# Kernel tuning notes

Measured on AMD Instinct MI355X. Metric: run time of the kernel, lower is better.

The kernel has to match this reference:

```python
import jax, jax.numpy as jnp
import numpy as np

N_TRAIN, N_FEAT, N_HID, ENC = 4096, 64, 256, 256
N_ANTES, ATT_H, MAX_LEN = 2048, 256, 16


def setup_inputs() -> dict:
    key = jax.random.key(0)
    ks = jax.random.split(key, 8)
    s = 0.05
    f32 = jnp.float32
    return {
        "context": jax.random.normal(ks[0], (N_TRAIN, N_FEAT), f32),
        "S": jax.random.uniform(ks[1], (N_TRAIN, N_ANTES), dtype=f32),
        "enc_w1": s * jax.random.normal(ks[2], (N_HID, N_FEAT), f32),
        "enc_b1": jnp.zeros((N_HID,), f32),
        "enc_w2": s * jax.random.normal(ks[3], (ENC, N_HID), f32),
        "enc_b2": jnp.zeros((ENC,), f32),
        "w_ih": s * jax.random.normal(ks[4], (4 * ENC, N_ANTES), f32),
        "w_hh": s * jax.random.normal(ks[5], (4 * ENC, ENC), f32),
        "b_ih": jnp.zeros((4 * ENC,), f32),
        "b_hh": jnp.zeros((4 * ENC,), f32),
        "att_w1": s * jax.random.normal(ks[6], (ATT_H, N_TRAIN + ENC), f32),
        "att_b1": jnp.zeros((ATT_H,), f32),
        "att_w2": s * jax.random.normal(ks[7], (1, ATT_H), f32),
        "att_b2": jnp.zeros((1,), f32),
    }


def _forward(context, S, enc_w1, enc_b1, enc_w2, enc_b2,
             w_ih, w_hh, b_ih, b_hh, att_w1, att_b1, att_w2, att_b2):
    n_train, n_antes = S.shape
    # context encoder: Linear -> ReLU -> Linear, initializes LSTM hidden state
    phi = jax.nn.relu(context @ enc_w1.T + enc_b1) @ enc_w2.T + enc_b2  # [n_train, ENC]
    # attention first layer split: columns [:n_train] act on S.T rows, rest on e_t
    Wa, Wb = att_w1[:, :n_train], att_w1[:, n_train:]
    pre = S.T @ Wa.T  # [n_antes, ATT_H], constant across timesteps
    bias = b_ih + b_hh
    x0 = jnp.ones((n_train, n_antes), S.dtype)

    def step(carry, _):
        h, c, x = carry
        # one LSTM cell step (PyTorch gate order i, f, g, o)
        z = x @ w_ih.T + h @ w_hh.T + bias  # [n_train, 4*ENC]
        i, f, g, o = jnp.split(z, 4, axis=-1)
        c = jax.nn.sigmoid(f) * c + jax.nn.sigmoid(i) * jnp.tanh(g)
        h = jax.nn.sigmoid(o) * jnp.tanh(c)
        e_t = h.mean(axis=0)  # mean over n_train (torch e.mean(1) on [1,n_train,H])
        hid = jax.nn.relu(pre + e_t @ Wb.T + att_b1)  # [n_antes, ATT_H]
        scores = (hid @ att_w2.T + att_b2)[:, 0]      # [n_antes]
        logp = jax.nn.log_softmax(scores, axis=0)
        idx = jnp.argmax(logp)
        # next input: chosen antecedent column broadcast across all antecedents
        x_next = jnp.broadcast_to(S[:, idx][:, None], (n_train, n_antes))
        return (h, c, x_next), logp

    _, d = jax.lax.scan(jax.checkpoint(step), (phi, jnp.zeros_like(phi), x0),
                        None, length=MAX_LEN)
    return d  # [MAX_LEN, n_antes] == torch cat(...).transpose(0, 1)


def reference(context, S, enc_w1, enc_b1, enc_w2, enc_b2,
              w_ih, w_hh, b_ih, b_hh, att_w1, att_b1, att_w2, att_b2):
    return _forward(context, S, enc_w1, enc_b1, enc_w2, enc_b2,
                    w_ih, w_hh, b_ih, b_hh, att_w1, att_b1, att_w2, att_b2)
```

## Files before the change

kernel.cpp:

```cpp
#include <hip/hip_runtime.h>
#include <hip/hip_bf16.h>
#include <math.h>

#define N_TRAIN 4096
#define N_FEAT  64
#define N_HID   256
#define ENC     256
#define N_ANTES 2048
#define ATT_H   256
#define MAX_LEN 16

typedef unsigned int u32;
typedef unsigned short u16;
typedef short short8 __attribute__((ext_vector_type(8)));
typedef float floatx16 __attribute__((ext_vector_type(16)));

__device__ __forceinline__ float fsig(float x)  { return 1.f / (1.f + __expf(-x)); }
__device__ __forceinline__ float ftanh(float x) { return 2.f / (1.f + __expf(-2.f * x)) - 1.f; }

__device__ __forceinline__ u16 f2bf(float x) {
    u32 b = __float_as_uint(x);
    return (u16)((b + 0x7FFFu + ((b >> 16) & 1u)) >> 16);
}
__device__ __forceinline__ float bf2f(u16 h) {
    return __uint_as_float(((u32)h) << 16);
}
__device__ __forceinline__ void split_bf(float v, u16& hi, u16& lo) {
    u32 b = __float_as_uint(v);
    hi = (u16)(b >> 16);
    float r = v - __uint_as_float(b & 0xFFFF0000u);
    lo = (u16)(__float_as_uint(r) >> 16);
}

__device__ __forceinline__ int kin_of(int l, int j) {
    return ((l >> 5) << 2) + (j & 3) + ((j >> 2) << 3);
}

template <bool RELU>
__global__ __launch_bounds__(256) void gemm_abT(
    const float* __restrict__ A, const float* __restrict__ B,
    const float* __restrict__ bias, float* __restrict__ C,
    int M, int N, int K, int lda, int ldb, int ldc)
{
    __shared__ __align__(16) float As[16][68];
    __shared__ __align__(16) float Bs[16][68];
    const int tid = threadIdx.x;
    const int m0 = blockIdx.x * 64, n0 = blockIdx.y * 64;
    const int tx = tid & 15, ty = tid >> 4;
    const int kl = tid & 15, rl = tid >> 4;
    float acc[4][4] = {};

    for (int k0 = 0; k0 < K; k0 += 16) {
        #pragma unroll
        for (int pp = 0; pp < 4; ++pp) {
            int r = rl + pp * 16;
            As[kl][r] = A[(size_t)(m0 + r) * lda + k0 + kl];
            Bs[kl][r] = B[(size_t)(n0 + r) * ldb + k0 + kl];
        }
        __syncthreads();
        #pragma unroll
        for (int k = 0; k < 16; ++k) {
            float4 av = *(const float4*)&As[k][ty * 4];
            float4 bv = *(const float4*)&Bs[k][tx * 4];
            float a4[4] = {av.x, av.y, av.z, av.w};
            float b4[4] = {bv.x, bv.y, bv.z, bv.w};
            #pragma unroll
            for (int i = 0; i < 4; ++i)
                #pragma unroll
                for (int j = 0; j < 4; ++j)
                    acc[i][j] = fmaf(a4[i], b4[j], acc[i][j]);
        }
        __syncthreads();
    }
    #pragma unroll
    for (int i = 0; i < 4; ++i) {
        int m = m0 + ty * 4 + i;
        #pragma unroll
        for (int j = 0; j < 4; ++j) {
            int n = n0 + tx * 4 + j;
            float v = acc[i][j] + bias[n];
            if (RELU) v = fmaxf(v, 0.f);
            C[(size_t)m * ldc + n] = v;
        }
    }
}

__global__ __launch_bounds__(256) void k_rowsum(const float* __restrict__ w_ih,
                                                float* __restrict__ rowsum)
{
    __shared__ float red[256];
    const int j = blockIdx.x, tid = threadIdx.x;
    float s = 0.f;
    for (int i = tid; i < N_ANTES; i += 256) s += w_ih[(size_t)j * N_ANTES + i];
    red[tid] = s; __syncthreads();
    for (int off = 128; off > 0; off >>= 1) {
        if (tid < off) red[tid] += red[tid + off];
        __syncthreads();
    }
    if (tid == 0) rowsum[j] = red[0];
}

__global__ __launch_bounds__(256) void k_wbT(const float* __restrict__ att_w1,
                                             float* __restrict__ WbT)
{
    int gid = blockIdx.x * 256 + threadIdx.x;
    int j = gid >> 8, k = gid & 255;
    WbT[(size_t)k * 256 + j] = att_w1[(size_t)j * (N_TRAIN + ENC) + N_TRAIN + k];
}

__global__ __launch_bounds__(256) void k_packAf(const float* __restrict__ att_w1,
                                                u16* __restrict__ Af_hi,
                                                u16* __restrict__ Af_lo)
{
    int gid = blockIdx.x * 256 + threadIdx.x;
    int j  = gid & 7;
    int l  = (gid >> 3) & 63;
    int kt = (gid >> 9) & 255;
    int mt = gid >> 17;
    int m = mt * 32 + (l & 31);
    int k = kt * 16 + kin_of(l, j);
    float v = att_w1[(size_t)m * (N_TRAIN + ENC) + k];
    u16 hi, lo; split_bf(v, hi, lo);
    Af_hi[gid] = hi;
    Af_lo[gid] = lo;
}

#define PSPLIT 4
__global__ __launch_bounds__(256) void k_gemm_preT(
    const u16* __restrict__ Af_hi, const u16* __restrict__ Af_lo,
    const float* __restrict__ S, float* __restrict__ P)
{
    const int tid = threadIdx.x, lane = tid & 63, w = tid >> 6;
    const int kz = blockIdx.x;
    const int np = blockIdx.y;
    const int mq = blockIdx.z;
    const int mt = mq * 2 + (w & 1);
    const int ni = w >> 1;
    const int nb = np * 64 + ni * 32 + (lane & 31);
    const int kb = 4 * (lane >> 5);
    floatx16 acc = {0,0,0,0,0,0,0,0,0,0,0,0,0,0,0,0};

    const int kt_beg = kz * 64, kt_end = kt_beg + 64;
    #pragma unroll 4
    for (int kt = kt_beg; kt < kt_end; ++kt) {
        size_t ao = (((size_t)mt * 256 + kt) * 64 + lane) * 8;
        short8 ahi = *(const short8*)(Af_hi + ao);
        short8 alo = *(const short8*)(Af_lo + ao);
        short8 bhi, blo;
        #pragma unroll
        for (int j = 0; j < 8; ++j) {
            int k = kt * 16 + kb + (j & 3) + 8 * (j >> 2);
            float v = S[(size_t)k * N_ANTES + nb];
            u16 hi, lo; split_bf(v, hi, lo);
            bhi[j] = (short)hi;
            blo[j] = (short)lo;
        }
        acc = __builtin_amdgcn_mfma_f32_32x32x16_bf16(ahi, bhi, acc, 0, 0, 0);
        acc = __builtin_amdgcn_mfma_f32_32x32x16_bf16(ahi, blo, acc, 0, 0, 0);
        acc = __builtin_amdgcn_mfma_f32_32x32x16_bf16(alo, bhi, acc, 0, 0, 0);
    }

    float* Pk = P + (size_t)kz * (ATT_H * N_ANTES);
    #pragma unroll
    for (int q = 0; q < 16; ++q) {
        int row = mt * 32 + (q & 3) + 8 * (q >> 2) + 4 * (lane >> 5);
        Pk[(size_t)row * N_ANTES + nb] = acc[q];
    }
}

__global__ __launch_bounds__(256) void k_reduce4(const float* __restrict__ P,
                                                 float* __restrict__ preT)
{
    int gid = blockIdx.x * 256 + threadIdx.x;
    const int SZ = ATT_H * N_ANTES;
    preT[gid] = (P[gid] + P[gid + SZ]) + (P[gid + 2 * SZ] + P[gid + 3 * SZ]);
}

__global__ __launch_bounds__(256) void k_packWf(const float* __restrict__ w_hh,
                                                u16* __restrict__ Wf_hi,
                                                u16* __restrict__ Wf_lo)
{
    int gid = blockIdx.x * 256 + threadIdx.x;
    int j    = gid & 7;
    int l    = (gid >> 3) & 63;
    int kt   = (gid >> 9) & 15;
    int nsub = (gid >> 13) & 1;
    int cb   = gid >> 14;
    int k  = kt * 16 + kin_of(l, j);
    int cc = nsub * 32 + (l & 31);
    int jj = cb * 16 + (cc >> 2);
    int g  = cc & 3;
    int J  = g * 256 + jj;
    float v = w_hh[(size_t)J * 256 + k];
    u16 hi = f2bf(v);
    Wf_hi[gid] = hi;
    Wf_lo[gid] = f2bf(v - bf2f(hi));
}

__global__ __launch_bounds__(256) void k_packHf(const float* __restrict__ h,
                                                u16* __restrict__ Hf_hi,
                                                u16* __restrict__ Hf_lo)
{
    int gid = blockIdx.x * 256 + threadIdx.x;
    int j  = gid & 7;
    int l  = (gid >> 3) & 63;
    int kt = (gid >> 9) & 15;
    int mt = gid >> 13;
    int m = mt * 32 + (l & 31);
    int k = kt * 16 + kin_of(l, j);
    float v = h[(size_t)m * 256 + k];
    u16 hi = f2bf(v);
    Hf_hi[gid] = hi;
    Hf_lo[gid] = f2bf(v - bf2f(hi));
}

__global__ __launch_bounds__(256) void k_zgemm(
    const u16* __restrict__ Hf_hi_r, const u16* __restrict__ Hf_lo_r,
    u16* __restrict__ Hf_hi_w, u16* __restrict__ Hf_lo_w,
    const u16* __restrict__ Wf_hi, const u16* __restrict__ Wf_lo,
    float* __restrict__ c,
    const float* __restrict__ rowsum, const float* __restrict__ b_ih,
    const float* __restrict__ b_hh, const float* __restrict__ S,
    const int* __restrict__ idx_buf, int t, float* __restrict__ e_acc_t)
{
    __shared__ __align__(16) float z_lds[128][68];
    __shared__ float red[256];
    const int tid  = threadIdx.x;
    const int lane = tid & 63;
    const int msub = tid >> 6;
    const int rb = blockIdx.x;
    const int cb = blockIdx.y;
    const int mt = rb * 4 + msub;

    floatx16 acc0 = {0,0,0,0,0,0,0,0,0,0,0,0,0,0,0,0};
    floatx16 acc1 = {0,0,0,0,0,0,0,0,0,0,0,0,0,0,0,0};
    const size_t aoff  = (size_t)mt * 16 * 512 + lane * 8;
    const size_t boff0 = (size_t)(cb * 2 + 0) * 16 * 512 + lane * 8;
    const size_t boff1 = (size_t)(cb * 2 + 1) * 16 * 512 + lane * 8;

    #pragma unroll 4
    for (int kt = 0; kt < 16; ++kt) {
        short8 ahi = *(const short8*)(Hf_hi_r + aoff  + kt * 512);
        short8 alo = *(const short8*)(Hf_lo_r + aoff  + kt * 512);
        short8 b0h = *(const short8*)(Wf_hi   + boff0 + kt * 512);
        short8 b0l = *(const short8*)(Wf_lo   + boff0 + kt * 512);
        short8 b1h = *(const short8*)(Wf_hi   + boff1 + kt * 512);
        short8 b1l = *(const short8*)(Wf_lo   + boff1 + kt * 512);
        acc0 = __builtin_amdgcn_mfma_f32_32x32x16_bf16(ahi, b0h, acc0, 0, 0, 0);
        acc0 = __builtin_amdgcn_mfma_f32_32x32x16_bf16(ahi, b0l, acc0, 0, 0, 0);
        acc0 = __builtin_amdgcn_mfma_f32_32x32x16_bf16(alo, b0h, acc0, 0, 0, 0);
        acc1 = __builtin_amdgcn_mfma_f32_32x32x16_bf16(ahi, b1h, acc1, 0, 0, 0);
        acc1 = __builtin_amdgcn_mfma_f32_32x32x16_bf16(ahi, b1l, acc1, 0, 0, 0);
        acc1 = __builtin_amdgcn_mfma_f32_32x32x16_bf16(alo, b1h, acc1, 0, 0, 0);
    }

    #pragma unroll
    for (int q = 0; q < 16; ++q) {
        int row = msub * 32 + (q & 3) + 8 * (q >> 2) + 4 * (lane >> 5);
        z_lds[row][lane & 31]        = acc0[q];
        z_lds[row][32 + (lane & 31)] = acc1[q];
    }
    __syncthreads();

    const int jj_l = tid & 15, rg = tid >> 4;
    const int Jc = cb * 16 + jj_l;
    float rs[4], bs[4];
    #pragma unroll
    for (int g = 0; g < 4; ++g) {
        int J = g * 256 + Jc;
        rs[g] = rowsum[J];
        bs[g] = b_ih[J] + b_hh[J];
    }
    const int idxp = (t > 0) ? idx_buf[t - 1] : 0;
    float esum = 0.f;
    #pragma unroll
    for (int p = 0; p < 8; ++p) {
        int r = rg * 8 + p;
        int rglob = rb * 128 + r;
        float a = (t > 0) ? S[(size_t)rglob * N_ANTES + idxp] : 1.f;
        float4 z4 = *(const float4*)&z_lds[r][jj_l * 4];
        float zi = z4.x + fmaf(a, rs[0], bs[0]);
        float zf = z4.y + fmaf(a, rs[1], bs[1]);
        float zg = z4.z + fmaf(a, rs[2], bs[2]);
        float zo = z4.w + fmaf(a, rs[3], bs[3]);
        size_t coff = (size_t)rglob * 256 + Jc;
        float cn = fsig(zf) * c[coff] + fsig(zi) * ftanh(zg);
        float hn = fsig(zo) * ftanh(cn);
        c[coff] = cn;
        esum += hn;
        u16 hi = f2bf(hn);
        u16 lo = f2bf(hn - bf2f(hi));
        int mtw    = rglob >> 5;
        int lane_a = (rglob & 31) + 32 * ((Jc >> 2) & 1);
        int ktw    = Jc >> 4;
        int jw     = (Jc & 3) + ((Jc >> 3) & 1) * 4;
        size_t off = (((size_t)mtw * 16 + ktw) * 64 + lane_a) * 8 + jw;
        Hf_hi_w[off] = hi;
        Hf_lo_w[off] = lo;
    }
    red[tid] = esum;
    __syncthreads();
    if (tid < 16) {
        float s = 0.f;
        #pragma unroll
        for (int q = 0; q < 16; ++q) s += red[tid + q * 16];
        atomicAdd(&e_acc_t[Jc - jj_l + tid], s);
    }
}

__global__ __launch_bounds__(256) void k_att(
    const float* __restrict__ preT, const float* __restrict__ e_accum_t,
    const float* __restrict__ WbT, const float* __restrict__ att_b1,
    const float* __restrict__ att_w2, const float* __restrict__ att_b2,
    float* __restrict__ scores, float* __restrict__ out_t,
    int* __restrict__ idx_t, int* __restrict__ cnt)
{
    __shared__ float e_lds[256];
    __shared__ float u[256];
    __shared__ float w2s[256];
    __shared__ float red[256];
    const int tid = threadIdx.x;
    e_lds[tid] = e_accum_t[tid] * (1.f / (float)N_TRAIN);
    w2s[tid] = att_w2[tid];
    __syncthreads();

    float uacc = att_b1[tid];
    for (int k = 0; k < 256; ++k)
        uacc = fmaf(e_lds[k], WbT[(size_t)k * 256 + tid], uacc);
    u[tid] = uacc;
    __syncthreads();

    const int pl = tid & 31, jq = tid >> 5;
    const int p = blockIdx.x * 32 + pl;
    float sc = 0.f;
    #pragma unroll 4
    for (int j = jq; j < 256; j += 8) {
        float v = preT[(size_t)j * N_ANTES + p] + u[j];
        sc = fmaf(fmaxf(v, 0.f), w2s[j], sc);
    }
    red[tid] = sc;
    __syncthreads();
    if (tid < 32) {
        float s = att_b2[0];
        #pragma unroll
        for (int q = 0; q < 8; ++q) s += red[tid + q * 32];
        scores[blockIdx.x * 32 + tid] = s;
    }

    __threadfence();
    __syncthreads();
    __shared__ int is_last;
    if (tid == 0)
        is_last = (atomicAdd(cnt, 1) == (int)gridDim.x - 1);
    __syncthreads();
    if (!is_last) return;
    __threadfence();

    __shared__ float smax[256];
    __shared__ int   sidx[256];
    __shared__ float ssum[256];

    float sv[8];
    #pragma unroll
    for (int i = 0; i < 8; ++i) sv[i] = scores[tid * 8 + i];

    float lmax = -INFINITY; int lidx = 0;
    #pragma unroll
    for (int i = 0; i < 8; ++i)
        if (sv[i] > lmax) { lmax = sv[i]; lidx = tid * 8 + i; }
    smax[tid] = lmax; sidx[tid] = lidx;
    __syncthreads();
    for (int off = 128; off > 0; off >>= 1) {
        if (tid < off) {
            float ov = smax[tid + off]; int oi = sidx[tid + off];
            if (ov > smax[tid] || (ov == smax[tid] && oi < sidx[tid])) {
                smax[tid] = ov; sidx[tid] = oi;
            }
        }
        __syncthreads();
    }
    const float gmax = smax[0];
    const int gidx = sidx[0];

    float lsum = 0.f;
    #pragma unroll
    for (int i = 0; i < 8; ++i) lsum += __expf(sv[i] - gmax);
    ssum[tid] = lsum;
    __syncthreads();
    for (int off = 128; off > 0; off >>= 1) {
        if (tid < off) ssum[tid] += ssum[tid + off];
        __syncthreads();
    }
    const float lse = gmax + logf(ssum[0]);

    #pragma unroll
    for (int i = 0; i < 8; ++i)
        out_t[tid * 8 + i] = sv[i] - lse;
    if (tid == 0) {
        idx_t[0] = gidx;
        *cnt = 0;
    }
}

extern "C" void kernel_launch(void* const* d_in, const int* in_sizes, int n_in,
                              void* d_out, int out_size, void* d_ws, size_t ws_size,
                              hipStream_t stream)
{
    (void)in_sizes; (void)n_in; (void)out_size; (void)ws_size;
    const float* context = (const float*)d_in[0];
    const float* S       = (const float*)d_in[1];
    const float* enc_w1  = (const float*)d_in[2];
    const float* enc_b1  = (const float*)d_in[3];
    const float* enc_w2  = (const float*)d_in[4];
    const float* enc_b2  = (const float*)d_in[5];
    const float* w_ih    = (const float*)d_in[6];
    const float* w_hh    = (const float*)d_in[7];
    const float* b_ih    = (const float*)d_in[8];
    const float* b_hh    = (const float*)d_in[9];
    const float* att_w1  = (const float*)d_in[10];
    const float* att_b1  = (const float*)d_in[11];
    const float* att_w2  = (const float*)d_in[12];
    const float* att_b2  = (const float*)d_in[13];
    float* out = (float*)d_out;
    float* ws  = (float*)d_ws;

    float* P      = ws;
    float* h_fp32 = ws;
    float* c      = ws + 1048576;
    float* hid1   = ws + 2097152;
    float* preT   = ws + 3145728;
    u16* Af_hi  = (u16*)(ws + 2097152);
    u16* Af_lo  = (u16*)(ws + 2621440);
    u16* Hf_hi1 = (u16*)(ws + 0);
    u16* Hf_lo1 = (u16*)(ws + 524288);
    u16* Hf_hi0 = (u16*)(ws + 2097152);
    u16* Hf_lo0 = (u16*)(ws + 2621440);
    u16* Wf_hi  = (u16*)(ws + 3670016);
    u16* Wf_lo  = (u16*)(ws + 3801088);
    int*   cnt    = (int*)(ws + 4718592);
    float* rowsum = ws + 4984832;
    float* e_acc  = ws + 4985856;
    float* scores = ws + 4989952;
    float* WbT    = ws + 4992000;
    int*   idxbuf = (int*)(ws + 5057536);

    k_rowsum<<<1024, 256, 0, stream>>>(w_ih, rowsum);
    k_wbT<<<256, 256, 0, stream>>>(att_w1, WbT);
    k_packWf<<<1024, 256, 0, stream>>>(w_hh, Wf_hi, Wf_lo);

    k_packAf<<<4096, 256, 0, stream>>>(att_w1, Af_hi, Af_lo);
    dim3 gp(PSPLIT, N_ANTES / 64, 4);
    k_gemm_preT<<<gp, 256, 0, stream>>>(Af_hi, Af_lo, S, P);
    k_reduce4<<<(ATT_H * N_ANTES) / 256, 256, 0, stream>>>(P, preT);

    hipMemsetAsync(c, 0, (size_t)N_TRAIN * ENC * sizeof(float), stream);
    hipMemsetAsync(e_acc, 0, (size_t)MAX_LEN * ENC * sizeof(float), stream);
    hipMemsetAsync(cnt, 0, sizeof(int), stream);

    dim3 g1(N_TRAIN / 64, N_HID / 64);
    gemm_abT<true><<<g1, 256, 0, stream>>>(context, enc_w1, enc_b1, hid1,
                                           N_TRAIN, N_HID, N_FEAT, N_FEAT, N_FEAT, N_HID);
    dim3 g2(N_TRAIN / 64, ENC / 64);
    gemm_abT<false><<<g2, 256, 0, stream>>>(hid1, enc_w2, enc_b2, h_fp32,
                                            N_TRAIN, ENC, N_HID, N_HID, N_HID, ENC);
    k_packHf<<<4096, 256, 0, stream>>>(h_fp32, Hf_hi0, Hf_lo0);

    dim3 gz(32, 16);
    for (int t = 0; t < MAX_LEN; ++t) {
        const u16 *hr, *lr; u16 *hw, *lw;
        if ((t & 1) == 0) { hr = Hf_hi0; lr = Hf_lo0; hw = Hf_hi1; lw = Hf_lo1; }
        else              { hr = Hf_hi1; lr = Hf_lo1; hw = Hf_hi0; lw = Hf_lo0; }
        k_zgemm<<<gz, 256, 0, stream>>>(hr, lr, hw, lw, Wf_hi, Wf_lo, c,
                                        rowsum, b_ih, b_hh, S, idxbuf, t,
                                        e_acc + t * 256);
        k_att<<<N_ANTES / 32, 256, 0, stream>>>(preT, e_acc + t * 256, WbT,
                                                att_b1, att_w2, att_b2, scores,
                                                out + t * N_ANTES, idxbuf + t, cnt);
    }
}
```

Before: 704.5 us.

## Split preT GEMM K over more blocks and halve zgemm block tile

The preT GEMM now splits K eight ways instead of four. Pairs of K slices accumulate with float atomics into the four partial buffers, which are zeroed by a new memset. The per-step LSTM gate GEMM kernel now gives each block 64 rows instead of 128, with each wave computing one 32x32 tile, and the grid is doubled to 64x16. Both changes aim to raise the number of workgroups and improve occupancy across the CUs, at the cost of atomic traffic, an extra memset, and more repeated loads of the shared weight tiles.

```diff
diff --git a/kernel.cpp b/kernel.cpp
--- a/kernel.cpp
+++ b/kernel.cpp
@@ -125,7 +125,7 @@
     Af_lo[gid] = lo;
 }
 
-#define PSPLIT 4
+#define PSPLIT 8
 __global__ __launch_bounds__(256) void k_gemm_preT(
     const u16* __restrict__ Af_hi, const u16* __restrict__ Af_lo,
     const float* __restrict__ S, float* __restrict__ P)
@@ -140,7 +140,7 @@
     const int kb = 4 * (lane >> 5);
     floatx16 acc = {0,0,0,0,0,0,0,0,0,0,0,0,0,0,0,0};
 
-    const int kt_beg = kz * 64, kt_end = kt_beg + 64;
+    const int kt_beg = kz * 32, kt_end = kt_beg + 32;
     #pragma unroll 4
     for (int kt = kt_beg; kt < kt_end; ++kt) {
         size_t ao = (((size_t)mt * 256 + kt) * 64 + lane) * 8;
@@ -160,11 +160,11 @@
         acc = __builtin_amdgcn_mfma_f32_32x32x16_bf16(alo, bhi, acc, 0, 0, 0);
     }
 
-    float* Pk = P + (size_t)kz * (ATT_H * N_ANTES);
+    float* Pk = P + (size_t)(kz & 3) * (ATT_H * N_ANTES);
     #pragma unroll
     for (int q = 0; q < 16; ++q) {
         int row = mt * 32 + (q & 3) + 8 * (q >> 2) + 4 * (lane >> 5);
-        Pk[(size_t)row * N_ANTES + nb] = acc[q];
+        atomicAdd(&Pk[(size_t)row * N_ANTES + nb], acc[q]);
     }
 }
 
@@ -223,42 +223,35 @@
     const float* __restrict__ b_hh, const float* __restrict__ S,
     const int* __restrict__ idx_buf, int t, float* __restrict__ e_acc_t)
 {
-    __shared__ __align__(16) float z_lds[128][68];
+    __shared__ __align__(16) float z_lds[64][68];
     __shared__ float red[256];
     const int tid  = threadIdx.x;
     const int lane = tid & 63;
-    const int msub = tid >> 6;
+    const int w    = tid >> 6;
     const int rb = blockIdx.x;
     const int cb = blockIdx.y;
-    const int mt = rb * 4 + msub;
-
-    floatx16 acc0 = {0,0,0,0,0,0,0,0,0,0,0,0,0,0,0,0};
-    floatx16 acc1 = {0,0,0,0,0,0,0,0,0,0,0,0,0,0,0,0};
-    const size_t aoff  = (size_t)mt * 16 * 512 + lane * 8;
-    const size_t boff0 = (size_t)(cb * 2 + 0) * 16 * 512 + lane * 8;
-    const size_t boff1 = (size_t)(cb * 2 + 1) * 16 * 512 + lane * 8;
+    const int mt = rb * 2 + (w & 1);
+    const int ni = w >> 1;
+
+    floatx16 acc = {0,0,0,0,0,0,0,0,0,0,0,0,0,0,0,0};
+    const size_t aoff = (size_t)mt * 16 * 512 + lane * 8;
+    const size_t boff = (size_t)(cb * 2 + ni) * 16 * 512 + lane * 8;
 
     #pragma unroll 4
     for (int kt = 0; kt < 16; ++kt) {
-        short8 ahi = *(const short8*)(Hf_hi_r + aoff  + kt * 512);
-        short8 alo = *(const short8*)(Hf_lo_r + aoff  + kt * 512);
-        short8 b0h = *(const short8*)(Wf_hi   + boff0 + kt * 512);
-        short8 b0l = *(const short8*)(Wf_lo   + boff0 + kt * 512);
-        short8 b1h = *(const short8*)(Wf_hi   + boff1 + kt * 512);
-        short8 b1l = *(const short8*)(Wf_lo   + boff1 + kt * 512);
-        acc0 = __builtin_amdgcn_mfma_f32_32x32x16_bf16(ahi, b0h, acc0, 0, 0, 0);
-        acc0 = __builtin_amdgcn_mfma_f32_32x32x16_bf16(ahi, b0l, acc0, 0, 0, 0);
-        acc0 = __builtin_amdgcn_mfma_f32_32x32x16_bf16(alo, b0h, acc0, 0, 0, 0);
-        acc1 = __builtin_amdgcn_mfma_f32_32x32x16_bf16(ahi, b1h, acc1, 0, 0, 0);
-        acc1 = __builtin_amdgcn_mfma_f32_32x32x16_bf16(ahi, b1l, acc1, 0, 0, 0);
-        acc1 = __builtin_amdgcn_mfma_f32_32x32x16_bf16(alo, b1h, acc1, 0, 0, 0);
+        short8 ahi = *(const short8*)(Hf_hi_r + aoff + kt * 512);
+        short8 alo = *(const short8*)(Hf_lo_r + aoff + kt * 512);
+        short8 bhi = *(const short8*)(Wf_hi   + boff + kt * 512);
+        short8 blo = *(const short8*)(Wf_lo   + boff + kt * 512);
+        acc = __builtin_amdgcn_mfma_f32_32x32x16_bf16(ahi, bhi, acc, 0, 0, 0);
+        acc = __builtin_amdgcn_mfma_f32_32x32x16_bf16(ahi, blo, acc, 0, 0, 0);
+        acc = __builtin_amdgcn_mfma_f32_32x32x16_bf16(alo, bhi, acc, 0, 0, 0);
     }
 
     #pragma unroll
     for (int q = 0; q < 16; ++q) {
-        int row = msub * 32 + (q & 3) + 8 * (q >> 2) + 4 * (lane >> 5);
-        z_lds[row][lane & 31]        = acc0[q];
-        z_lds[row][32 + (lane & 31)] = acc1[q];
+        int row = (w & 1) * 32 + (q & 3) + 8 * (q >> 2) + 4 * (lane >> 5);
+        z_lds[row][ni * 32 + (lane & 31)] = acc[q];
     }
     __syncthreads();
 
@@ -274,9 +267,9 @@
     const int idxp = (t > 0) ? idx_buf[t - 1] : 0;
     float esum = 0.f;
     #pragma unroll
-    for (int p = 0; p < 8; ++p) {
-        int r = rg * 8 + p;
-        int rglob = rb * 128 + r;
+    for (int p = 0; p < 4; ++p) {
+        int r = rg * 4 + p;
+        int rglob = rb * 64 + r;
         float a = (t > 0) ? S[(size_t)rglob * N_ANTES + idxp] : 1.f;
         float4 z4 = *(const float4*)&z_lds[r][jj_l * 4];
         float zi = z4.x + fmaf(a, rs[0], bs[0]);
@@ -449,6 +442,7 @@
     k_packWf<<<1024, 256, 0, stream>>>(w_hh, Wf_hi, Wf_lo);
 
     k_packAf<<<4096, 256, 0, stream>>>(att_w1, Af_hi, Af_lo);
+    hipMemsetAsync(P, 0, (size_t)4 * ATT_H * N_ANTES * sizeof(float), stream);
     dim3 gp(PSPLIT, N_ANTES / 64, 4);
     k_gemm_preT<<<gp, 256, 0, stream>>>(Af_hi, Af_lo, S, P);
     k_reduce4<<<(ATT_H * N_ANTES) / 256, 256, 0, stream>>>(P, preT);
@@ -465,7 +459,7 @@
                                             N_TRAIN, ENC, N_HID, N_HID, N_HID, ENC);
     k_packHf<<<4096, 256, 0, stream>>>(h_fp32, Hf_hi0, Hf_lo0);
 
-    dim3 gz(32, 16);
+    dim3 gz(64, 16);
     for (int t = 0; t < MAX_LEN; ++t) {
         const u16 *hr, *lr; u16 *hw, *lw;
         if ((t & 1) == 0) { hr = Hf_hi0; lr = Hf_lo0; hw = Hf_hi1; lw = Hf_lo1; }
```

Result: no change. 694.4 us (-1.4%).
